# Kernel optimization log

Measured on AMD Instinct MI355X. Metric: run time of the kernel, lower is better.

The kernel has to match this reference:

```python
import jax, jax.numpy as jnp
from jax import lax
import numpy as np

KK = 9          # 3x3 kernel points
BN_EPS = 1e-5


def setup_inputs() -> dict:
    key = jax.random.key(0)
    ks = jax.random.split(key, 8)
    B, C, O, H, W = 4, 256, 256, 64, 64
    x = jax.random.normal(ks[0], (B, C, H, W), jnp.float32)
    # offset/mask conv: 27 = 2*9 offsets + 9 mask logits; small init so offsets are O(1) px
    w_off = jax.random.normal(ks[1], (3 * KK, C, 3, 3), jnp.float32) * 0.01
    b_off = jnp.zeros((3 * KK,), jnp.float32)
    # main deformable conv weight [O, C, 3, 3]
    w = jax.random.normal(ks[2], (O, C, 3, 3), jnp.float32) * (1.0 / np.sqrt(C * KK))
    b = jax.random.normal(ks[3], (O,), jnp.float32) * 0.01
    # BatchNorm (eval mode) params
    gamma = jax.random.uniform(ks[4], (O,), jnp.float32, 0.5, 1.5)
    beta = jax.random.normal(ks[5], (O,), jnp.float32) * 0.1
    running_mean = jax.random.normal(ks[6], (O,), jnp.float32) * 0.1
    running_var = jax.random.uniform(ks[7], (O,), jnp.float32, 0.5, 1.5)
    return dict(x=x, w_off=w_off, b_off=b_off, w=w, b=b, gamma=gamma,
                beta=beta, running_mean=running_mean, running_var=running_var)


def _bilinear_sample(x, py, px):
    """x: [B,C,H,W]; py/px: [B,KK,H,W] float sample coords -> [B,C,KK,H,W]."""
    B, C, H, W = x.shape
    xflat = x.reshape(B, C, H * W)
    y0 = jnp.floor(py)
    x0 = jnp.floor(px)
    ly = py - y0      # frac weights
    lx = px - x0
    y0i = y0.astype(jnp.int32)
    x0i = x0.astype(jnp.int32)

    def corner(yi, xi, wgt):
        valid = (yi >= 0) & (yi < H) & (xi >= 0) & (xi < W)  # zero padding outside
        idx = jnp.clip(yi, 0, H - 1) * W + jnp.clip(xi, 0, W - 1)
        v = jnp.take_along_axis(xflat, idx.reshape(B, 1, -1), axis=2)  # [B,C,KK*H*W]
        return v * (wgt * valid).reshape(B, 1, -1)

    out = (corner(y0i,     x0i,     (1 - ly) * (1 - lx))
           + corner(y0i,     x0i + 1, (1 - ly) * lx)
           + corner(y0i + 1, x0i,     ly * (1 - lx))
           + corner(y0i + 1, x0i + 1, ly * lx))
    return out.reshape(B, C, KK, H, W)


def _deform_conv_bn_relu(x, w_off, b_off, w, b, gamma, beta, running_mean, running_var):
    B, C, H, W = x.shape
    O = w.shape[0]
    # offset/mask branch: plain 3x3 conv, stride 1, pad 1
    om = lax.conv_general_dilated(x, w_off, (1, 1), [(1, 1), (1, 1)])
    om = om + b_off[None, :, None, None]              # [B, 27, H, W]
    off_y = om[:, :KK]                                # DCNv2: o1 -> y offsets
    off_x = om[:, KK:2 * KK]                          # o2 -> x offsets
    mask = jax.nn.sigmoid(om[:, 2 * KK:])             # [B, 9, H, W]

    # base sampling grid for each of the 9 kernel taps (stride 1, pad 1)
    k = jnp.arange(KK)
    ki = (k // 3)[None, :, None, None].astype(jnp.float32)
    kj = (k % 3)[None, :, None, None].astype(jnp.float32)
    hh = jnp.arange(H, dtype=jnp.float32)[None, None, :, None]
    ww = jnp.arange(W, dtype=jnp.float32)[None, None, None, :]
    py = hh - 1.0 + ki + off_y                        # [B,9,H,W]
    px = ww - 1.0 + kj + off_x

    sampled = _bilinear_sample(x, py, px)             # [B,C,9,H,W]
    sampled = sampled * mask[:, None]                 # modulated (DCNv2)

    out = jnp.einsum('bckhw,ock->bohw', sampled, w.reshape(O, C, KK))
    out = out + b[None, :, None, None]

    # BatchNorm (eval / running stats) + ReLU
    inv = gamma / jnp.sqrt(running_var + BN_EPS)
    out = out * inv[None, :, None, None] + (beta - running_mean * inv)[None, :, None, None]
    return jax.nn.relu(out)


def reference(x, w_off, b_off, w, b, gamma, beta, running_mean, running_var):
    return _deform_conv_bn_relu(x, w_off, b_off, w, b, gamma, beta,
                                running_mean, running_var)
```

## Files before the change

### kernel.cpp

```cpp
#include <hip/hip_runtime.h>

#define HH 64
#define WWD 64
#define CIN 256
#define OUTC 256
#define BB 4
#define KK 9
#define NSO2 18
#define QOFF 4
#define NITH 20
#define WROWS 8
#define WPIX 512

typedef __attribute__((ext_vector_type(8))) short short8;
typedef __attribute__((ext_vector_type(4))) short short4v;
typedef __attribute__((ext_vector_type(4))) unsigned short ushort4v;
typedef __attribute__((ext_vector_type(4))) float float4v;

__device__ __forceinline__ short f2bf(float f) {
    unsigned u = __builtin_bit_cast(unsigned, f);
    u += 0x7fffu + ((u >> 16) & 1u);
    return (short)(u >> 16);
}
__device__ __forceinline__ float bf2f(short s) {
    unsigned u = ((unsigned)(unsigned short)s) << 16;
    return __builtin_bit_cast(float, u);
}
__device__ __forceinline__ int div9(int s) { return (s * 57) >> 9; }

__global__ __launch_bounds__(256) void k_packs(const float* __restrict__ w,
                                               const float* __restrict__ w_off,
                                               short* __restrict__ wt2,
                                               short* __restrict__ wo2) {
    const int bid = blockIdx.x;
    if (bid < 2304) {
        int gid = bid * 256 + threadIdx.x;
        int kk = gid & 31;
        int o  = (gid >> 5) & 255;
        int s  = gid >> 13;
        int chunk = div9(s), tap = s - 9 * chunk;
        int c = (chunk << 5) + kk;
        wt2[gid] = f2bf(w[(o * CIN + c) * 9 + tap]);
    } else {
        int gid = (bid - 2304) * 256 + threadIdx.x;
        int kk = gid & 31;
        int m  = (gid >> 5) & 31;
        int s  = gid >> 10;
        int chunk = div9(s), tap = s - 9 * chunk;
        int c = (chunk << 5) + kk;
        wo2[gid] = (m < 27) ? f2bf(w_off[(m * CIN + c) * 9 + tap]) : (short)0;
    }
}

__global__ __launch_bounds__(256) void k_off_mfma(const float* __restrict__ x,
                                                  const short* __restrict__ wo2,
                                                  float* __restrict__ om_part) {
    const int wgid = blockIdx.x;
    const int swz  = ((wgid & 7) << 7) + (wgid >> 3);
    const int q = swz & 3;
    const int h = (swz >> 2) & 63;
    const int b = swz >> 8;
    const int tid = threadIdx.x;
    const int lane = tid & 63;
    const int wid  = tid >> 6;

    __shared__ short S[2][4][64][8];

    const int px_t = tid & 63;
    const int g    = tid >> 6;
    const float* xb = x + ((size_t)b << 20);

    float gv[8];
    auto ISSUE = [&](int s2) {
        const int chunk = div9(s2), tap = s2 - 9 * chunk;
        const int gy = h + tap / 3 - 1;
        const int gx = px_t + tap % 3 - 1;
        const bool ok = ((unsigned)gy < 64u) && ((unsigned)gx < 64u);
        const float* xc = xb + (((chunk << 5) + (g << 3)) << 12) + (gy << 6) + gx;
#pragma unroll
        for (int j = 0; j < 8; ++j)
            gv[j] = ok ? xc[(size_t)j << 12] : 0.f;
    };
    auto CONSUME = [&](int buf) {
        short8 p;
#pragma unroll
        for (int j = 0; j < 8; ++j) p[j] = f2bf(gv[j]);
        *(short8*)(&S[buf][g][px_t][0]) = p;
    };

    const int arow = lane & 15;
    const int akk  = (lane >> 4) << 3;
    const int bpx  = lane & 15;
    const int bg   = lane >> 4;

    float4v acc0 = {0.f, 0.f, 0.f, 0.f};
    float4v acc1 = {0.f, 0.f, 0.f, 0.f};

    const int s0 = q * NSO2;
    ISSUE(s0); CONSUME(0); ISSUE(s0 + 1);
    const short* abase = wo2 + (size_t)s0 * 1024 + arow * 32 + akk;
    short8 aC0 = *(const short8*)(abase);
    short8 aC1 = *(const short8*)(abase + 512);
    __syncthreads();

#pragma unroll 1
    for (int ls = 0; ls < NSO2; ++ls) {
        const int lsn = (ls + 1 < NSO2) ? ls + 1 : ls;
        const short* an = wo2 + (size_t)(s0 + lsn) * 1024 + arow * 32 + akk;
        short8 aN0 = *(const short8*)(an);
        short8 aN1 = *(const short8*)(an + 512);

        short8 bf = *(const short8*)(&S[ls & 1][bg][(wid << 4) + bpx][0]);
        acc0 = __builtin_amdgcn_mfma_f32_16x16x32_bf16(aC0, bf, acc0, 0, 0, 0);
        acc1 = __builtin_amdgcn_mfma_f32_16x16x32_bf16(aC1, bf, acc1, 0, 0, 0);

        if (ls < NSO2 - 1) {
            CONSUME((ls + 1) & 1);
            if (ls + 2 < NSO2) ISSUE(s0 + ls + 2);
        }
        aC0 = aN0; aC1 = aN1;
        __syncthreads();
    }

    const int pxo = (wid << 4) + bpx;
    float* ob = om_part + (((size_t)(q * BB + b) * 27) << 12) + (h << 6) + pxo;
#pragma unroll
    for (int r = 0; r < 4; ++r) {
        const int m0 = ((lane >> 4) << 2) + r;
        ob[(size_t)m0 << 12] = acc0[r];
        const int m1 = 16 + m0;
        if (m1 < 27) ob[(size_t)m1 << 12] = acc1[r];
    }
}

__global__ __launch_bounds__(512) void k_main(
    const float* __restrict__ x, const float* __restrict__ om_part,
    const float* __restrict__ b_off, const short* __restrict__ wt2,
    float* __restrict__ outr, float* __restrict__ part1) {

    const int wgid = blockIdx.x;
    const int swz  = ((wgid & 7) << 6) + (wgid >> 3);
    const int q = swz & 1;
    const int h = (swz >> 1) & 63;
    const int b = swz >> 7;
    const int tid  = threadIdx.x;
    const int lane = tid & 63;
    const int wid  = tid >> 6;

    __shared__ ushort4v sidx2[576];
    __shared__ ushort4v sw4[576];
    __shared__ short    S[2][2][4][64][8];
    __shared__ short    xw[WPIX * 32];

    for (int j = tid; j < 576; j += 512) {
        const int k  = j >> 6;
        const int px = j & 63;
        const int sp = (h << 6) + px;
        float oy = b_off[k], ox = b_off[k + KK], mz = b_off[k + 2 * KK];
#pragma unroll
        for (int qq = 0; qq < QOFF; ++qq) {
            const float* bp = om_part + (size_t)((qq * BB + b) * 27) * 4096 + sp;
            oy += bp[k * 4096];
            ox += bp[(k + KK) * 4096];
            mz += bp[(k + 2 * KK) * 4096];
        }
        const float mask = 1.f / (1.f + expf(-mz));
        const float py  = (float)h  - 1.f + (float)(k / 3) + oy;
        const float pxc = (float)px - 1.f + (float)(k % 3) + ox;
        const float y0f = floorf(py), x0f = floorf(pxc);
        const float ly = py - y0f, lx = pxc - x0f;
        const int y0 = (int)y0f, x0 = (int)x0f;

        float w00, w01, w10, w11;
        {
            bool v = (y0 >= 0) && (y0 < HH) && (x0 >= 0) && (x0 < WWD);
            w00 = v ? (1.f - ly) * (1.f - lx) * mask : 0.f;
        }
        {
            bool v = (y0 >= 0) && (y0 < HH) && (x0 + 1 < WWD) && (x0 + 1 >= 0);
            w01 = v ? (1.f - ly) * lx * mask : 0.f;
        }
        {
            bool v = (y0 + 1 >= 0) && (y0 + 1 < HH) && (x0 >= 0) && (x0 < WWD);
            w10 = v ? ly * (1.f - lx) * mask : 0.f;
        }
        {
            bool v = (y0 + 1 >= 0) && (y0 + 1 < HH) && (x0 + 1 >= 0) && (x0 + 1 < WWD);
            w11 = v ? ly * lx * mask : 0.f;
        }
        const int cy0 = min(max(y0, 0), 63),     cy1 = min(max(y0 + 1, 0), 63);
        const int cx0 = min(max(x0, 0), 63),     cx1 = min(max(x0 + 1, 0), 63);
        const int li0 = cy0 - (h - 3),           li1 = cy1 - (h - 3);
        ushort4v pv;
        if ((unsigned)li0 < (unsigned)WROWS && (unsigned)li1 < (unsigned)WROWS) {
            const int p00 = (li0 << 6) + cx0, p01 = (li0 << 6) + cx1;
            const int p10 = (li1 << 6) + cx0, p11 = (li1 << 6) + cx1;
            pv.x = (unsigned short)((p00 << 6) | ((p00 + (p00 >> 2)) & 3));
            pv.y = (unsigned short)((p01 << 6) | ((p01 + (p01 >> 2)) & 3));
            pv.z = (unsigned short)((p10 << 6) | ((p10 + (p10 >> 2)) & 3));
            pv.w = (unsigned short)((p11 << 6) | ((p11 + (p11 >> 2)) & 3));
        } else {
            pv.x = 0xFFFFu;
            pv.y = (unsigned short)(y0 + 32);
            pv.z = (unsigned short)(x0 + 32);
            pv.w = 0;
        }
        ushort4v wv;
        wv.x = (unsigned short)f2bf(w00);
        wv.y = (unsigned short)f2bf(w01);
        wv.z = (unsigned short)f2bf(w10);
        wv.w = (unsigned short)f2bf(w11);
        sidx2[j] = pv;
        sw4[j]   = wv;
    }

    const float* xb = x + ((size_t)b << 20);

    auto STAGE = [&](int chunk) {
#pragma unroll
        for (int r4 = 0; r4 < 4; ++r4) {
            const int t   = r4 * 512 + tid;
            const int g   = t >> 9;
            const int pix = t & 511;
            const int wr  = pix >> 6, col = pix & 63;
            const int gro = (min(max(h - 3 + wr, 0), 63) << 6) + col;
            const float* xc = xb + ((size_t)((chunk << 5) + (g << 3)) << 12) + gro;
            short8 p;
#pragma unroll
            for (int j = 0; j < 8; ++j) p[j] = f2bf(xc[(size_t)j << 12]);
            const int pos = (g + pix + (pix >> 2)) & 3;
            *(short8*)&xw[pix * 32 + pos * 8] = p;
        }
    };

    auto SAMPLE = [&](int c2, int sub2, int ntaps2, int buf2) {
        const int tp = tid >> 8;
        if (tp < ntaps2) {
            const int slot = tid & 255;
            const int g  = slot >> 6;
            const int px = slot & 63;
            const int tap = sub2 * 2 + tp;
            const int j = (tap << 6) + px;
            const ushort4v sv = sidx2[j];
            const ushort4v wv = sw4[j];
            const float w00 = bf2f((short)wv.x), w01 = bf2f((short)wv.y);
            const float w10 = bf2f((short)wv.z), w11 = bf2f((short)wv.w);
            float a[8];
            if (sv.x != 0xFFFFu) {
                const int o0 = ((sv.x & 0xFFC0u) >> 1) + (((sv.x + g) & 3u) << 3);
                const int o1 = ((sv.y & 0xFFC0u) >> 1) + (((sv.y + g) & 3u) << 3);
                const int o2 = ((sv.z & 0xFFC0u) >> 1) + (((sv.z + g) & 3u) << 3);
                const int o3 = ((sv.w & 0xFFC0u) >> 1) + (((sv.w + g) & 3u) << 3);
                const short8 c00 = *(const short8*)&xw[o0];
                const short8 c01 = *(const short8*)&xw[o1];
                const short8 c10 = *(const short8*)&xw[o2];
                const short8 c11 = *(const short8*)&xw[o3];
#pragma unroll
                for (int j2 = 0; j2 < 8; ++j2)
                    a[j2] = w00 * bf2f(c00[j2]) + w01 * bf2f(c01[j2])
                          + w10 * bf2f(c10[j2]) + w11 * bf2f(c11[j2]);
            } else {
                const int y0 = (int)sv.y - 32, x0 = (int)sv.z - 32;
                const int cy0 = min(max(y0, 0), 63), cy1 = min(max(y0 + 1, 0), 63);
                const int cx0 = min(max(x0, 0), 63), cx1 = min(max(x0 + 1, 0), 63);
                const int i00 = (cy0 << 6) + cx0, i01 = (cy0 << 6) + cx1;
                const int i10 = (cy1 << 6) + cx0, i11 = (cy1 << 6) + cx1;
                const float* xc = xb + ((size_t)((c2 << 5) + (g << 3)) << 12);
#pragma unroll
                for (int j2 = 0; j2 < 8; ++j2) {
                    a[j2] = w00 * xc[i00] + w01 * xc[i01]
                          + w10 * xc[i10] + w11 * xc[i11];
                    xc += 4096;
                }
            }
            short8 rr;
#pragma unroll
            for (int j2 = 0; j2 < 8; ++j2) rr[j2] = f2bf(a[j2]);
            *(short8*)&S[buf2][tp][g][px][0] = rr;
        }
    };

    const short* wbase = wt2 + ((wid * 32 + (lane & 15)) << 5) + ((lane >> 4) << 3);
    const int bpx = lane & 15;
    const int bg  = lane >> 4;

    float4v acc[2][4];
#pragma unroll
    for (int mt = 0; mt < 2; ++mt)
#pragma unroll
        for (int nt = 0; nt < 4; ++nt) acc[mt][nt] = (float4v){0.f, 0.f, 0.f, 0.f};

    const int c0 = q * 4;
    const int sA0 = c0 * 9;

    __syncthreads();
    STAGE(c0);
    __syncthreads();
    SAMPLE(c0, 0, 2, 0);
    short8 aC00 = *(const short8*)(wbase + (size_t)sA0 * 8192);
    short8 aC01 = *(const short8*)(wbase + (size_t)sA0 * 8192 + 512);
    short8 aC10 = *(const short8*)(wbase + (size_t)(sA0 + 1) * 8192);
    short8 aC11 = *(const short8*)(wbase + (size_t)(sA0 + 1) * 8192 + 512);
    __syncthreads();

    int c = c0, sub = 0;
#pragma unroll 1
    for (int it = 0; it < NITH; ++it) {
        const int ntaps = (sub < 4) ? 2 : 1;
        int subn = sub + 1, cn = c;
        if (subn == 5) { subn = 0; cn = c + 1; }
        const int ntapsN = (subn < 4) ? 2 : 1;
        const int sN = cn * 9 + subn * 2;

        short8 aN00 = aC00, aN01 = aC01, aN10 = aC10, aN11 = aC11;
        if (it + 1 < NITH) {
            aN00 = *(const short8*)(wbase + (size_t)sN * 8192);
            aN01 = *(const short8*)(wbase + (size_t)sN * 8192 + 512);
            if (ntapsN == 2) {
                aN10 = *(const short8*)(wbase + (size_t)(sN + 1) * 8192);
                aN11 = *(const short8*)(wbase + (size_t)(sN + 1) * 8192 + 512);
            }
        }

        const int buf = it & 1;
        __builtin_amdgcn_s_setprio(1);
        {
            const short* Sb = &S[buf][0][bg][bpx][0];
            short8 b0 = *(const short8*)(Sb);
            short8 b1 = *(const short8*)(Sb + 128);
            short8 b2 = *(const short8*)(Sb + 256);
            short8 b3 = *(const short8*)(Sb + 384);
            acc[0][0] = __builtin_amdgcn_mfma_f32_16x16x32_bf16(aC00, b0, acc[0][0], 0, 0, 0);
            acc[0][1] = __builtin_amdgcn_mfma_f32_16x16x32_bf16(aC00, b1, acc[0][1], 0, 0, 0);
            acc[0][2] = __builtin_amdgcn_mfma_f32_16x16x32_bf16(aC00, b2, acc[0][2], 0, 0, 0);
            acc[0][3] = __builtin_amdgcn_mfma_f32_16x16x32_bf16(aC00, b3, acc[0][3], 0, 0, 0);
            acc[1][0] = __builtin_amdgcn_mfma_f32_16x16x32_bf16(aC01, b0, acc[1][0], 0, 0, 0);
            acc[1][1] = __builtin_amdgcn_mfma_f32_16x16x32_bf16(aC01, b1, acc[1][1], 0, 0, 0);
            acc[1][2] = __builtin_amdgcn_mfma_f32_16x16x32_bf16(aC01, b2, acc[1][2], 0, 0, 0);
            acc[1][3] = __builtin_amdgcn_mfma_f32_16x16x32_bf16(aC01, b3, acc[1][3], 0, 0, 0);
        }
        if (ntaps == 2) {
            const short* Sb = &S[buf][1][bg][bpx][0];
            short8 b0 = *(const short8*)(Sb);
            short8 b1 = *(const short8*)(Sb + 128);
            short8 b2 = *(const short8*)(Sb + 256);
            short8 b3 = *(const short8*)(Sb + 384);
            acc[0][0] = __builtin_amdgcn_mfma_f32_16x16x32_bf16(aC10, b0, acc[0][0], 0, 0, 0);
            acc[0][1] = __builtin_amdgcn_mfma_f32_16x16x32_bf16(aC10, b1, acc[0][1], 0, 0, 0);
            acc[0][2] = __builtin_amdgcn_mfma_f32_16x16x32_bf16(aC10, b2, acc[0][2], 0, 0, 0);
            acc[0][3] = __builtin_amdgcn_mfma_f32_16x16x32_bf16(aC10, b3, acc[0][3], 0, 0, 0);
            acc[1][0] = __builtin_amdgcn_mfma_f32_16x16x32_bf16(aC11, b0, acc[1][0], 0, 0, 0);
            acc[1][1] = __builtin_amdgcn_mfma_f32_16x16x32_bf16(aC11, b1, acc[1][1], 0, 0, 0);
            acc[1][2] = __builtin_amdgcn_mfma_f32_16x16x32_bf16(aC11, b2, acc[1][2], 0, 0, 0);
            acc[1][3] = __builtin_amdgcn_mfma_f32_16x16x32_bf16(aC11, b3, acc[1][3], 0, 0, 0);
        }
        __builtin_amdgcn_s_setprio(0);

        if (it + 1 < NITH) {
            if (sub == 4) {
                STAGE(cn);
                __syncthreads();
            }
            SAMPLE(cn, subn, ntapsN, (it + 1) & 1);
        }
        aC00 = aN00; aC01 = aN01; aC10 = aN10; aC11 = aN11;
        __syncthreads();
        c = cn; sub = subn;
    }

    const int r4 = lane >> 4;
    float* ob = (q == 0 ? outr : part1) + (((size_t)b * 256) << 12) + (h << 6);
#pragma unroll
    for (int mt = 0; mt < 2; ++mt)
#pragma unroll
        for (int nt = 0; nt < 4; ++nt) {
            const int px = nt * 16 + bpx;
#pragma unroll
            for (int r = 0; r < 4; ++r) {
                const int o = wid * 32 + mt * 16 + r4 * 4 + r;
                ob[((size_t)o << 12) + px] = acc[mt][nt][r];
            }
        }
}

__global__ __launch_bounds__(256) void k_bn(const float* __restrict__ part1,
                                            const float* __restrict__ bias,
                                            const float* __restrict__ gamma,
                                            const float* __restrict__ beta,
                                            const float* __restrict__ rmean,
                                            const float* __restrict__ rvar,
                                            float* __restrict__ out) {
    const int NTOT4 = BB * OUTC * 4096 / 4;
    int i = blockIdx.x * 256 + threadIdx.x;
    const int stride = gridDim.x * 256;
#pragma unroll 1
    for (; i < NTOT4; i += stride) {
        const int e0 = i << 2;
        const int o  = (e0 >> 12) & 255;
        const float inv = gamma[o] * rsqrtf(rvar[o] + 1e-5f);
        const float sh  = beta[o] - rmean[o] * inv + bias[o] * inv;
        float4 a = ((const float4*)out)[i];
        float4 p = ((const float4*)part1)[i];
        float4 v;
        v.x = fmaxf((a.x + p.x) * inv + sh, 0.f);
        v.y = fmaxf((a.y + p.y) * inv + sh, 0.f);
        v.z = fmaxf((a.z + p.z) * inv + sh, 0.f);
        v.w = fmaxf((a.w + p.w) * inv + sh, 0.f);
        ((float4*)out)[i] = v;
    }
}

extern "C" void kernel_launch(void* const* d_in, const int* in_sizes, int n_in,
                              void* d_out, int out_size, void* d_ws, size_t ws_size,
                              hipStream_t stream) {
    const float* x     = (const float*)d_in[0];
    const float* w_off = (const float*)d_in[1];
    const float* b_off = (const float*)d_in[2];
    const float* w     = (const float*)d_in[3];
    const float* bias  = (const float*)d_in[4];
    const float* gamma = (const float*)d_in[5];
    const float* beta  = (const float*)d_in[6];
    const float* rmean = (const float*)d_in[7];
    const float* rvar  = (const float*)d_in[8];
    float* out = (float*)d_out;

    float* om_part = (float*)d_ws;
    short* wt2     = (short*)(om_part + QOFF * BB * 27 * 4096);
    short* wo2     = wt2 + 72 * 256 * 32;
    float* part1   = (float*)(wo2 + 72 * 32 * 32);

    k_packs<<<2592, 256, 0, stream>>>(w, w_off, wt2, wo2);
    k_off_mfma<<<1024, 256, 0, stream>>>(x, wo2, om_part);
    k_main<<<512, 512, 0, stream>>>(x, om_part, b_off, wt2, out, part1);
    k_bn<<<2048, 256, 0, stream>>>(part1, bias, gamma, beta, rmean, rvar, out);
}
```

Measured before the change: 73.84 us.

## Double k_main block to 1024 threads and pack bf16 with v_cvt_pk_bf16_f32

k_main now launches 1024 threads per block. Each wave computes 16 output channels instead of 32, which halves the accumulators and A-fragment registers per wave and gives each block twice as many waves to hide latency. Staging is done in two passes instead of four. All float-to-bf16 conversions now use the packed hardware instruction v_cvt_pk_bf16_f32 in place of the manual round-to-nearest bit arithmetic. Risks are a tighter per-thread register budget under the new launch bounds and more barrier cost with a larger block.

New measurement: 106.6 us. 1.44x slower.

```diff
diff --git a/kernel.cpp b/kernel.cpp
--- a/kernel.cpp
+++ b/kernel.cpp
@@ -25,6 +25,17 @@
 __device__ __forceinline__ float bf2f(short s) {
     unsigned u = ((unsigned)(unsigned short)s) << 16;
     return __builtin_bit_cast(float, u);
+}
+__device__ __forceinline__ unsigned cvtpk(float a, float b) {
+    unsigned r;
+    asm("v_cvt_pk_bf16_f32 %0, %1, %2" : "=v"(r) : "v"(a), "v"(b));
+    return r;
+}
+__device__ __forceinline__ short8 pack8(const float* a) {
+    union { short8 s; unsigned u[4]; } r;
+    r.u[0] = cvtpk(a[0], a[1]); r.u[1] = cvtpk(a[2], a[3]);
+    r.u[2] = cvtpk(a[4], a[5]); r.u[3] = cvtpk(a[6], a[7]);
+    return r.s;
 }
 __device__ __forceinline__ int div9(int s) { return (s * 57) >> 9; }
 
@@ -82,9 +93,7 @@
             gv[j] = ok ? xc[(size_t)j << 12] : 0.f;
     };
     auto CONSUME = [&](int buf) {
-        short8 p;
-#pragma unroll
-        for (int j = 0; j < 8; ++j) p[j] = f2bf(gv[j]);
+        short8 p = pack8(gv);
         *(short8*)(&S[buf][g][px_t][0]) = p;
     };
 
@@ -133,7 +142,7 @@
     }
 }
 
-__global__ __launch_bounds__(512) void k_main(
+__global__ __launch_bounds__(1024, 8) void k_main(
     const float* __restrict__ x, const float* __restrict__ om_part,
     const float* __restrict__ b_off, const short* __restrict__ wt2,
     float* __restrict__ outr, float* __restrict__ part1) {
@@ -152,7 +161,8 @@
     __shared__ short    S[2][2][4][64][8];
     __shared__ short    xw[WPIX * 32];
 
-    for (int j = tid; j < 576; j += 512) {
+    if (tid < 576) {
+        const int j  = tid;
         const int k  = j >> 6;
         const int px = j & 63;
         const int sp = (h << 6) + px;
@@ -218,16 +228,17 @@
 
     auto STAGE = [&](int chunk) {
 #pragma unroll
-        for (int r4 = 0; r4 < 4; ++r4) {
-            const int t   = r4 * 512 + tid;
+        for (int r2 = 0; r2 < 2; ++r2) {
+            const int t   = r2 * 1024 + tid;
             const int g   = t >> 9;
             const int pix = t & 511;
             const int wr  = pix >> 6, col = pix & 63;
             const int gro = (min(max(h - 3 + wr, 0), 63) << 6) + col;
             const float* xc = xb + ((size_t)((chunk << 5) + (g << 3)) << 12) + gro;
-            short8 p;
-#pragma unroll
-            for (int j = 0; j < 8; ++j) p[j] = f2bf(xc[(size_t)j << 12]);
+            float a[8];
+#pragma unroll
+            for (int j = 0; j < 8; ++j) a[j] = xc[(size_t)j << 12];
+            short8 p = pack8(a);
             const int pos = (g + pix + (pix >> 2)) & 3;
             *(short8*)&xw[pix * 32 + pos * 8] = p;
         }
@@ -273,22 +284,18 @@
                     xc += 4096;
                 }
             }
-            short8 rr;
-#pragma unroll
-            for (int j2 = 0; j2 < 8; ++j2) rr[j2] = f2bf(a[j2]);
+            short8 rr = pack8(a);
             *(short8*)&S[buf2][tp][g][px][0] = rr;
         }
     };
 
-    const short* wbase = wt2 + ((wid * 32 + (lane & 15)) << 5) + ((lane >> 4) << 3);
+    const short* wbase = wt2 + ((wid * 16 + (lane & 15)) << 5) + ((lane >> 4) << 3);
     const int bpx = lane & 15;
     const int bg  = lane >> 4;
 
-    float4v acc[2][4];
-#pragma unroll
-    for (int mt = 0; mt < 2; ++mt)
-#pragma unroll
-        for (int nt = 0; nt < 4; ++nt) acc[mt][nt] = (float4v){0.f, 0.f, 0.f, 0.f};
+    float4v acc[4];
+#pragma unroll
+    for (int nt = 0; nt < 4; ++nt) acc[nt] = (float4v){0.f, 0.f, 0.f, 0.f};
 
     const int c0 = q * 4;
     const int sA0 = c0 * 9;
@@ -297,10 +304,8 @@
     STAGE(c0);
     __syncthreads();
     SAMPLE(c0, 0, 2, 0);
-    short8 aC00 = *(const short8*)(wbase + (size_t)sA0 * 8192);
-    short8 aC01 = *(const short8*)(wbase + (size_t)sA0 * 8192 + 512);
-    short8 aC10 = *(const short8*)(wbase + (size_t)(sA0 + 1) * 8192);
-    short8 aC11 = *(const short8*)(wbase + (size_t)(sA0 + 1) * 8192 + 512);
+    short8 aC0 = *(const short8*)(wbase + (size_t)sA0 * 8192);
+    short8 aC1 = *(const short8*)(wbase + (size_t)(sA0 + 1) * 8192);
     __syncthreads();
 
     int c = c0, sub = 0;
@@ -312,14 +317,11 @@
         const int ntapsN = (subn < 4) ? 2 : 1;
         const int sN = cn * 9 + subn * 2;
 
-        short8 aN00 = aC00, aN01 = aC01, aN10 = aC10, aN11 = aC11;
+        short8 aN0 = aC0, aN1 = aC1;
         if (it + 1 < NITH) {
-            aN00 = *(const short8*)(wbase + (size_t)sN * 8192);
-            aN01 = *(const short8*)(wbase + (size_t)sN * 8192 + 512);
-            if (ntapsN == 2) {
-                aN10 = *(const short8*)(wbase + (size_t)(sN + 1) * 8192);
-                aN11 = *(const short8*)(wbase + (size_t)(sN + 1) * 8192 + 512);
-            }
+            aN0 = *(const short8*)(wbase + (size_t)sN * 8192);
+            if (ntapsN == 2)
+                aN1 = *(const short8*)(wbase + (size_t)(sN + 1) * 8192);
         }
 
         const int buf = it & 1;
@@ -330,14 +332,10 @@
             short8 b1 = *(const short8*)(Sb + 128);
             short8 b2 = *(const short8*)(Sb + 256);
             short8 b3 = *(const short8*)(Sb + 384);
-            acc[0][0] = __builtin_amdgcn_mfma_f32_16x16x32_bf16(aC00, b0, acc[0][0], 0, 0, 0);
-            acc[0][1] = __builtin_amdgcn_mfma_f32_16x16x32_bf16(aC00, b1, acc[0][1], 0, 0, 0);
-            acc[0][2] = __builtin_amdgcn_mfma_f32_16x16x32_bf16(aC00, b2, acc[0][2], 0, 0, 0);
-            acc[0][3] = __builtin_amdgcn_mfma_f32_16x16x32_bf16(aC00, b3, acc[0][3], 0, 0, 0);
-            acc[1][0] = __builtin_amdgcn_mfma_f32_16x16x32_bf16(aC01, b0, acc[1][0], 0, 0, 0);
-            acc[1][1] = __builtin_amdgcn_mfma_f32_16x16x32_bf16(aC01, b1, acc[1][1], 0, 0, 0);
-            acc[1][2] = __builtin_amdgcn_mfma_f32_16x16x32_bf16(aC01, b2, acc[1][2], 0, 0, 0);
-            acc[1][3] = __builtin_amdgcn_mfma_f32_16x16x32_bf16(aC01, b3, acc[1][3], 0, 0, 0);
+            acc[0] = __builtin_amdgcn_mfma_f32_16x16x32_bf16(aC0, b0, acc[0], 0, 0, 0);
+            acc[1] = __builtin_amdgcn_mfma_f32_16x16x32_bf16(aC0, b1, acc[1], 0, 0, 0);
+            acc[2] = __builtin_amdgcn_mfma_f32_16x16x32_bf16(aC0, b2, acc[2], 0, 0, 0);
+            acc[3] = __builtin_amdgcn_mfma_f32_16x16x32_bf16(aC0, b3, acc[3], 0, 0, 0);
         }
         if (ntaps == 2) {
             const short* Sb = &S[buf][1][bg][bpx][0];
@@ -345,14 +343,10 @@
             short8 b1 = *(const short8*)(Sb + 128);
             short8 b2 = *(const short8*)(Sb + 256);
             short8 b3 = *(const short8*)(Sb + 384);
-            acc[0][0] = __builtin_amdgcn_mfma_f32_16x16x32_bf16(aC10, b0, acc[0][0], 0, 0, 0);
-            acc[0][1] = __builtin_amdgcn_mfma_f32_16x16x32_bf16(aC10, b1, acc[0][1], 0, 0, 0);
-            acc[0][2] = __builtin_amdgcn_mfma_f32_16x16x32_bf16(aC10, b2, acc[0][2], 0, 0, 0);
-            acc[0][3] = __builtin_amdgcn_mfma_f32_16x16x32_bf16(aC10, b3, acc[0][3], 0, 0, 0);
-            acc[1][0] = __builtin_amdgcn_mfma_f32_16x16x32_bf16(aC11, b0, acc[1][0], 0, 0, 0);
-            acc[1][1] = __builtin_amdgcn_mfma_f32_16x16x32_bf16(aC11, b1, acc[1][1], 0, 0, 0);
-            acc[1][2] = __builtin_amdgcn_mfma_f32_16x16x32_bf16(aC11, b2, acc[1][2], 0, 0, 0);
-            acc[1][3] = __builtin_amdgcn_mfma_f32_16x16x32_bf16(aC11, b3, acc[1][3], 0, 0, 0);
+            acc[0] = __builtin_amdgcn_mfma_f32_16x16x32_bf16(aC1, b0, acc[0], 0, 0, 0);
+            acc[1] = __builtin_amdgcn_mfma_f32_16x16x32_bf16(aC1, b1, acc[1], 0, 0, 0);
+            acc[2] = __builtin_amdgcn_mfma_f32_16x16x32_bf16(aC1, b2, acc[2], 0, 0, 0);
+            acc[3] = __builtin_amdgcn_mfma_f32_16x16x32_bf16(aC1, b3, acc[3], 0, 0, 0);
         }
         __builtin_amdgcn_s_setprio(0);
 
@@ -363,7 +357,7 @@
             }
             SAMPLE(cn, subn, ntapsN, (it + 1) & 1);
         }
-        aC00 = aN00; aC01 = aN01; aC10 = aN10; aC11 = aN11;
+        aC0 = aN0; aC1 = aN1;
         __syncthreads();
         c = cn; sub = subn;
     }
@@ -371,16 +365,14 @@
     const int r4 = lane >> 4;
     float* ob = (q == 0 ? outr : part1) + (((size_t)b * 256) << 12) + (h << 6);
 #pragma unroll
-    for (int mt = 0; mt < 2; ++mt)
-#pragma unroll
-        for (int nt = 0; nt < 4; ++nt) {
-            const int px = nt * 16 + bpx;
-#pragma unroll
-            for (int r = 0; r < 4; ++r) {
-                const int o = wid * 32 + mt * 16 + r4 * 4 + r;
-                ob[((size_t)o << 12) + px] = acc[mt][nt][r];
-            }
-        }
+    for (int nt = 0; nt < 4; ++nt) {
+        const int px = nt * 16 + bpx;
+#pragma unroll
+        for (int r = 0; r < 4; ++r) {
+            const int o = wid * 16 + r4 * 4 + r;
+            ob[((size_t)o << 12) + px] = acc[nt][r];
+        }
+    }
 }
 
 __global__ __launch_bounds__(256) void k_bn(const float* __restrict__ part1,
@@ -431,6 +423,6 @@
 
     k_packs<<<2592, 256, 0, stream>>>(w, w_off, wt2, wo2);
     k_off_mfma<<<1024, 256, 0, stream>>>(x, wo2, om_part);
-    k_main<<<512, 512, 0, stream>>>(x, om_part, b_off, wt2, out, part1);
+    k_main<<<512, 1024, 0, stream>>>(x, om_part, b_off, wt2, out, part1);
     k_bn<<<2048, 256, 0, stream>>>(part1, bias, gamma, beta, rmean, rvar, out);
 }
```
